# Kernel optimization log

Measured on AMD Instinct MI355X. Metric: run time of the kernel, lower is better.

The kernel has to match this reference:

```python
import jax, jax.numpy as jnp
import numpy as np

BATCH = 16384
NUM_FEATURES = 1024  # sum(field_dims)
CROSS_DIMS = NUM_FEATURES * (NUM_FEATURES - 1) // 2  # 523776


def setup_inputs() -> dict:
    key = jax.random.key(0)
    kx, kw = jax.random.split(key)
    x = jax.random.uniform(kx, (BATCH, NUM_FEATURES), dtype=jnp.float32)
    # xavier-uniform init of a (cross_dims, 1) parameter: bound = sqrt(6/(fan_in+fan_out))
    bound = float(np.sqrt(6.0 / (CROSS_DIMS + 1)))
    w = jax.random.uniform(kw, (CROSS_DIMS,), dtype=jnp.float32, minval=-bound, maxval=bound)
    return {"x": x, "w": w}


def reference(x, w):
    # POLY2: out_b = sigmoid( sum_{i<j} w_{ij} * x_{b,i} * x_{b,j} )
    # sklearn PolynomialFeatures(interaction_only) emits pairs in combinations
    # (row-major i<j) order, identical to triu_indices(k=1) ordering.
    F = x.shape[1]
    iu, ju = jnp.triu_indices(F, k=1)
    W = jnp.zeros((F, F), dtype=x.dtype).at[iu, ju].set(w)  # [F,F] strictly upper-tri
    # quadratic form without materializing the [B, F*(F-1)/2] pairwise matrix
    out = jnp.einsum('bi,ij,bj->b', x, W, x)  # [B]
    return jax.nn.sigmoid(out.astype(jnp.float32))
```

## Files before the change

kernel.cpp:

```cpp
#include <hip/hip_runtime.h>
#include <hip/hip_bf16.h>

#define F 1024
#define B_ROWS 16384

typedef short v8s __attribute__((ext_vector_type(8)));
typedef float v4f __attribute__((ext_vector_type(4)));
typedef unsigned short v8u __attribute__((ext_vector_type(8)));
typedef unsigned short ushort_t;

__device__ __forceinline__ unsigned short f2bf(float f) {
    unsigned int u = __builtin_bit_cast(unsigned int, f);
    u = (u + 0x7FFFu + ((u >> 16) & 1u)) >> 16;
    return (unsigned short)u;
}

__device__ __forceinline__ void gload_lds16(const ushort_t* g, ushort_t* l) {
    __builtin_amdgcn_global_load_lds(
        (const __attribute__((address_space(1))) unsigned int*)g,
        (__attribute__((address_space(3))) unsigned int*)l,
        16, 0, 0);
}


__global__ __launch_bounds__(256) void prep_kernel(
        const float* __restrict__ w, const float* __restrict__ x,
        ushort_t* __restrict__ Bp, ushort_t* __restrict__ Xp,
        float* __restrict__ acc) {
    const int bid  = blockIdx.x;
    const int tid  = threadIdx.x;
    const int lane = tid & 63;
    const int wave = tid >> 6;
    const int l16  = lane & 15;
    const int quad = lane >> 4;

    if (bid < 64) {
        acc[bid * 256 + tid] = 0.0f;
    } else if (bid < 576) {
        const int c  = (bid - 64) * 4 + wave;
        const int n  = (c >> 5) * 16 + l16;
        const int k0 = (c & 31) * 32 + quad * 8;
        v8u o;
#pragma unroll
        for (int e = 0; e < 8; ++e) {
            const int k = k0 + e;
            float v = 0.0f;
            if (k < n) {
                const int idx = k * (F - 1) - (k * (k - 1)) / 2 + (n - k - 1);
                v = w[idx];
            }
            o[e] = f2bf(v);
        }
        *(v8u*)(Bp + (size_t)c * 512 + lane * 8) = o;
    } else {
        const int c  = (bid - 576) * 4 + wave;
        const int r  = (c >> 5) * 16 + l16;
        const int k0 = (c & 31) * 32 + quad * 8;
        const float* src = x + (size_t)r * F + k0;
        float4 v0 = *(const float4*)(src);
        float4 v1 = *(const float4*)(src + 4);
        v8u o;
        o[0] = f2bf(v0.x); o[1] = f2bf(v0.y); o[2] = f2bf(v0.z); o[3] = f2bf(v0.w);
        o[4] = f2bf(v1.x); o[5] = f2bf(v1.y); o[6] = f2bf(v1.z); o[7] = f2bf(v1.w);
        *(v8u*)(Xp + (size_t)c * 512 + lane * 8) = o;
    }
}

__global__ __launch_bounds__(256, 3) void gemm_kernel(
        const ushort_t* __restrict__ Xp,
        const ushort_t* __restrict__ Bp,
        const float*   __restrict__ Xf,
        float*         __restrict__ rowacc) {
    __shared__ ushort_t Ls[2 * 16 * 512];

    const int f   = blockIdx.x;
    const int xcd = f & 7;
    const int g   = f >> 3;
    const int y   = g & 15;
    const int nt  = 7 - (g >> 4);
    const int blockM = (xcd * 16 + y) * 128;
    const int blockN = nt * 128;
    const int tEnd   = 4 * (nt + 1);

    const int tid   = threadIdx.x;
    const int lane  = tid & 63;
    const int wave  = tid >> 6;
    const int waveM = wave >> 1;
    const int waveN = wave & 1;
    const int quad  = lane >> 4;
    const int l16   = lane & 15;

    const int mgBase = blockM >> 4;
    const int ngB    = nt * 8;

    const bool stageA = (wave < 2);
    const int  qBase  = (wave & 1) * 4;
    const ushort_t* gsrc0 = stageA
        ? Xp + ((size_t)(mgBase + qBase) * 32) * 512
        : Bp + ((size_t)(ngB  + qBase) * 32) * 512;
    const int slot0 = (stageA ? 0 : 8) + qBase;

#define STAGE(t, buf)                                                          \
    {                                                                          \
        _Pragma("unroll")                                                      \
        for (int q = 0; q < 4; ++q) {                                          \
            gload_lds16(gsrc0 + ((size_t)q * 32 + (t)) * 512 + lane * 8,       \
                        Ls + ((buf) * 16 + slot0 + q) * 512);                  \
        }                                                                      \
    }

    v4f acc[4][4];
#pragma unroll
    for (int i = 0; i < 4; i++)
#pragma unroll
        for (int j = 0; j < 4; j++) acc[i][j] = (v4f)(0.0f);

    v8s afr[4], bfr[4];

    STAGE(0, 0)
    __syncthreads();

    for (int t = 0; t < tEnd; ++t) {
        const int  buf  = t & 1;
        const bool more = (t + 1 < tEnd);
        if (more) STAGE(t + 1, buf ^ 1)

#pragma unroll
        for (int mi = 0; mi < 4; ++mi)
            afr[mi] = *(const v8s*)(Ls + (buf * 16 + waveM * 4 + mi) * 512 + lane * 8);
#pragma unroll
        for (int ni = 0; ni < 4; ++ni)
            bfr[ni] = *(const v8s*)(Ls + (buf * 16 + 8 + waveN * 4 + ni) * 512 + lane * 8);

#pragma unroll
        for (int mi = 0; mi < 4; ++mi)
#pragma unroll
            for (int ni = 0; ni < 4; ++ni)
                acc[mi][ni] = __builtin_amdgcn_mfma_f32_16x16x32_bf16(
                    afr[mi], bfr[ni], acc[mi][ni], 0, 0, 0);

        if (more) __syncthreads();
    }
#undef STAGE

#pragma unroll
    for (int mi = 0; mi < 4; mi++) {
#pragma unroll
        for (int r = 0; r < 4; r++) {
            const int b = blockM + waveM * 64 + mi * 16 + quad * 4 + r;
            const float* xr = Xf + (size_t)b * F + blockN + waveN * 64 + l16;
            float pv = acc[mi][0][r] * xr[0]
                     + acc[mi][1][r] * xr[16]
                     + acc[mi][2][r] * xr[32]
                     + acc[mi][3][r] * xr[48];
            pv += __shfl_xor(pv, 1);
            pv += __shfl_xor(pv, 2);
            pv += __shfl_xor(pv, 4);
            pv += __shfl_xor(pv, 8);
            if (l16 == 0) atomicAdd(&rowacc[b], pv);
        }
    }
}

__global__ void sigmoid_kernel(const float* __restrict__ acc, float* __restrict__ out) {
    int b = blockIdx.x * blockDim.x + threadIdx.x;
    out[b] = 1.0f / (1.0f + __expf(-acc[b]));
}

__global__ void fallback_kernel(const float* __restrict__ x, const float* __restrict__ w,
                                float* __restrict__ out) {
    __shared__ float xs[F];
    __shared__ float partial[4];
    const int b = blockIdx.x;
    for (int i = threadIdx.x; i < F; i += 256) xs[i] = x[(size_t)b * F + i];
    __syncthreads();
    float s = 0.0f;
    for (int i = threadIdx.x; i < F - 1; i += 256) {
        const float xi = xs[i];
        const int kbase = i * (F - 1) - (i * (i - 1)) / 2 - i - 1;
        for (int j = i + 1; j < F; j++) s += w[kbase + j] * xi * xs[j];
    }
    for (int off = 32; off; off >>= 1) s += __shfl_down(s, off);
    if ((threadIdx.x & 63) == 0) partial[threadIdx.x >> 6] = s;
    __syncthreads();
    if (threadIdx.x == 0) {
        float t = partial[0] + partial[1] + partial[2] + partial[3];
        out[b] = 1.0f / (1.0f + __expf(-t));
    }
}

extern "C" void kernel_launch(void* const* d_in, const int* in_sizes, int n_in,
                              void* d_out, int out_size, void* d_ws, size_t ws_size,
                              hipStream_t stream) {
    const float* x = (const float*)d_in[0];
    const float* w = (const float*)d_in[1];
    float* out = (float*)d_out;

    const size_t acc_bytes = 65536;
    const size_t B_bytes   = (size_t)F * F * 2;
    const size_t Xp_bytes  = (size_t)B_ROWS * F * 2;
    const size_t needed = acc_bytes + B_bytes + Xp_bytes;

    if (ws_size < needed) {
        fallback_kernel<<<B_ROWS, 256, 0, stream>>>(x, w, out);
        return;
    }

    float*    acc = (float*)d_ws;
    ushort_t* Bp  = (ushort_t*)((char*)d_ws + acc_bytes);
    ushort_t* Xp  = (ushort_t*)((char*)d_ws + acc_bytes + B_bytes);

    prep_kernel<<<64 + 512 + 8192, 256, 0, stream>>>(w, x, Bp, Xp, acc);
    gemm_kernel<<<1024, 256, 0, stream>>>(Xp, Bp, x, acc);
    sigmoid_kernel<<<B_ROWS / 256, 256, 0, stream>>>(acc, out);
}
```

Before: 128.6 us.

## Fuse x bf16 conversion into GEMM by loading fp32 x directly into LDS

```diff
diff --git a/kernel.cpp b/kernel.cpp
--- a/kernel.cpp
+++ b/kernel.cpp
@@ -15,7 +15,14 @@
     return (unsigned short)u;
 }
 
-__device__ __forceinline__ void gload_lds16(const ushort_t* g, ushort_t* l) {
+__device__ __forceinline__ unsigned int cvtpk_bf16(float a, float b) {
+    __hip_bfloat162 h = __float22bfloat162_rn(make_float2(a, b));
+    unsigned int u;
+    __builtin_memcpy(&u, &h, 4);
+    return u;
+}
+
+__device__ __forceinline__ void gload16(const void* g, void* l) {
     __builtin_amdgcn_global_load_lds(
         (const __attribute__((address_space(1))) unsigned int*)g,
         (__attribute__((address_space(3))) unsigned int*)l,
@@ -24,8 +31,8 @@
 
 
 __global__ __launch_bounds__(256) void prep_kernel(
-        const float* __restrict__ w, const float* __restrict__ x,
-        ushort_t* __restrict__ Bp, ushort_t* __restrict__ Xp,
+        const float* __restrict__ w,
+        ushort_t* __restrict__ Bp,
         float* __restrict__ acc) {
     const int bid  = blockIdx.x;
     const int tid  = threadIdx.x;
@@ -36,7 +43,7 @@
 
     if (bid < 64) {
         acc[bid * 256 + tid] = 0.0f;
-    } else if (bid < 576) {
+    } else {
         const int c  = (bid - 64) * 4 + wave;
         const int n  = (c >> 5) * 16 + l16;
         const int k0 = (c & 31) * 32 + quad * 8;
@@ -52,26 +59,14 @@
             o[e] = f2bf(v);
         }
         *(v8u*)(Bp + (size_t)c * 512 + lane * 8) = o;
-    } else {
-        const int c  = (bid - 576) * 4 + wave;
-        const int r  = (c >> 5) * 16 + l16;
-        const int k0 = (c & 31) * 32 + quad * 8;
-        const float* src = x + (size_t)r * F + k0;
-        float4 v0 = *(const float4*)(src);
-        float4 v1 = *(const float4*)(src + 4);
-        v8u o;
-        o[0] = f2bf(v0.x); o[1] = f2bf(v0.y); o[2] = f2bf(v0.z); o[3] = f2bf(v0.w);
-        o[4] = f2bf(v1.x); o[5] = f2bf(v1.y); o[6] = f2bf(v1.z); o[7] = f2bf(v1.w);
-        *(v8u*)(Xp + (size_t)c * 512 + lane * 8) = o;
     }
 }
 
 __global__ __launch_bounds__(256, 3) void gemm_kernel(
-        const ushort_t* __restrict__ Xp,
         const ushort_t* __restrict__ Bp,
         const float*   __restrict__ Xf,
         float*         __restrict__ rowacc) {
-    __shared__ ushort_t Ls[2 * 16 * 512];
+    __shared__ char Ls[2 * 24 * 1024];
 
     const int f   = blockIdx.x;
     const int xcd = f & 7;
@@ -90,22 +85,23 @@
     const int quad  = lane >> 4;
     const int l16   = lane & 15;
 
-    const int mgBase = blockM >> 4;
-    const int ngB    = nt * 8;
-
-    const bool stageA = (wave < 2);
-    const int  qBase  = (wave & 1) * 4;
-    const ushort_t* gsrc0 = stageA
-        ? Xp + ((size_t)(mgBase + qBase) * 32) * 512
-        : Bp + ((size_t)(ngB  + qBase) * 32) * 512;
-    const int slot0 = (stageA ? 0 : 8) + qBase;
+    const int ngB = nt * 8;
 
 #define STAGE(t, buf)                                                          \
     {                                                                          \
         _Pragma("unroll")                                                      \
-        for (int q = 0; q < 4; ++q) {                                          \
-            gload_lds16(gsrc0 + ((size_t)q * 32 + (t)) * 512 + lane * 8,       \
-                        Ls + ((buf) * 16 + slot0 + q) * 512);                  \
+        for (int q = 0; q < 6; ++q) {                                          \
+            const int qq = wave * 6 + q;                                       \
+            if (qq < 16) {                                                     \
+                const int ac = qq >> 1, p = qq & 1;                            \
+                gload16(Xf + (size_t)(blockM + ac * 16 + l16) * F              \
+                            + (t) * 32 + quad * 8 + p * 4,                     \
+                        Ls + (buf) * 24576 + ac * 2048 + p * 1024);            \
+            } else {                                                           \
+                const int bc = qq - 16;                                        \
+                gload16(Bp + ((size_t)(ngB + bc) * 32 + (t)) * 512 + lane * 8, \
+                        Ls + (buf) * 24576 + 16384 + bc * 1024);               \
+            }                                                                  \
         }                                                                      \
     }
 
@@ -126,11 +122,21 @@
         if (more) STAGE(t + 1, buf ^ 1)
 
 #pragma unroll
-        for (int mi = 0; mi < 4; ++mi)
-            afr[mi] = *(const v8s*)(Ls + (buf * 16 + waveM * 4 + mi) * 512 + lane * 8);
+        for (int mi = 0; mi < 4; ++mi) {
+            const char* Ab = Ls + buf * 24576 + (waveM * 4 + mi) * 2048 + lane * 16;
+            v4f lo = *(const v4f*)(Ab);
+            v4f hi = *(const v4f*)(Ab + 1024);
+            uint4 pk;
+            pk.x = cvtpk_bf16(lo[0], lo[1]);
+            pk.y = cvtpk_bf16(lo[2], lo[3]);
+            pk.z = cvtpk_bf16(hi[0], hi[1]);
+            pk.w = cvtpk_bf16(hi[2], hi[3]);
+            afr[mi] = __builtin_bit_cast(v8s, pk);
+        }
 #pragma unroll
         for (int ni = 0; ni < 4; ++ni)
-            bfr[ni] = *(const v8s*)(Ls + (buf * 16 + 8 + waveN * 4 + ni) * 512 + lane * 8);
+            bfr[ni] = *(const v8s*)(Ls + buf * 24576 + 16384
+                                    + (waveN * 4 + ni) * 1024 + lane * 16);
 
 #pragma unroll
         for (int mi = 0; mi < 4; ++mi)
@@ -198,8 +204,7 @@
 
     const size_t acc_bytes = 65536;
     const size_t B_bytes   = (size_t)F * F * 2;
-    const size_t Xp_bytes  = (size_t)B_ROWS * F * 2;
-    const size_t needed = acc_bytes + B_bytes + Xp_bytes;
+    const size_t needed = acc_bytes + B_bytes;
 
     if (ws_size < needed) {
         fallback_kernel<<<B_ROWS, 256, 0, stream>>>(x, w, out);
@@ -208,9 +213,8 @@
 
     float*    acc = (float*)d_ws;
     ushort_t* Bp  = (ushort_t*)((char*)d_ws + acc_bytes);
-    ushort_t* Xp  = (ushort_t*)((char*)d_ws + acc_bytes + B_bytes);
-
-    prep_kernel<<<64 + 512 + 8192, 256, 0, stream>>>(w, x, Bp, Xp, acc);
-    gemm_kernel<<<1024, 256, 0, stream>>>(Xp, Bp, x, acc);
+
+    prep_kernel<<<64 + 512, 256, 0, stream>>>(w, Bp, acc);
+    gemm_kernel<<<1024, 256, 0, stream>>>(Bp, x, acc);
     sigmoid_kernel<<<B_ROWS / 256, 256, 0, stream>>>(acc, out);
 }
```

New measurement: 143.6 us. +11.6%, slower.
